# Performance work log

Hardware: AMD Instinct MI355X
Metric: run time of the kernel (lower is better)

The kernel has to match this reference:

```python
import jax, jax.numpy as jnp
import numpy as np

B, N, DIM, H, DH = 8, 1024, 512, 8, 64
INNER = H * DH
SCALE = DH ** -0.5


def setup_inputs() -> dict:
    key = jax.random.key(0)
    ks = jax.random.split(key, 9)
    s = 0.02
    return {
        "x": jax.random.normal(ks[0], (B, N, DIM), jnp.float32),
        "lidar": jax.random.normal(ks[1], (B, N, INNER), jnp.float32),
        "w_qkv": jax.random.normal(ks[2], (3 * INNER, DIM), jnp.float32) * s,
        "w_merge": jax.random.normal(ks[3], (DH, DH), jnp.float32) * s,
        "b_merge": jnp.zeros((DH,), jnp.float32),
        "w_out": jax.random.normal(ks[4], (DIM, INNER), jnp.float32) * s,
        "b_out": jnp.zeros((DIM,), jnp.float32),
        "conv_w": jax.random.normal(ks[5], (2,), jnp.float32) * 0.5,
        "conv_b": jnp.zeros((), jnp.float32),
    }


def _split_heads(t):  # [b, n, h*d] -> [b, h, n, d]
    b, n, _ = t.shape
    return t.reshape(b, n, H, DH).transpose(0, 2, 1, 3)


def reference(x, lidar, w_qkv, w_merge, b_merge, w_out, b_out, conv_w, conv_b):
    b, n, _ = x.shape
    qkv = x @ w_qkv.T  # [b, n, 3*inner]
    q, k, v = jnp.split(qkv, 3, axis=-1)
    q, k, v = _split_heads(q), _split_heads(k), _split_heads(v)
    lid = _split_heads(lidar)

    dots = jnp.einsum('bhid,bhjd->bhij', q, k) * SCALE
    lidar_sim = jnp.einsum('bhid,bhjd->bhij', lid, lid) * SCALE
    lidar_sim = jax.nn.softmax(lidar_sim, axis=-1)

    # 1x1 conv over 2 channels == learned linear blend of the two score maps
    mid = conv_w[0] * dots + conv_w[1] * lidar_sim + conv_b
    attn = jax.nn.softmax(mid, axis=-1)

    out = jnp.einsum('bhij,bhjd->bhid', attn, v)
    out = out @ w_merge.T + b_merge                  # per-head linear_merge
    out = out.transpose(0, 2, 1, 3).reshape(b, n, INNER)  # b h n d -> b n (h d)
    out = out @ w_out.T + b_out                      # to_out (dropout = identity)
    return (out, lidar)
```

## Files before the change

kernel.cpp:

```cpp
#include <hip/hip_runtime.h>
#include <hip/hip_bf16.h>

#define B_      8
#define N_      1024
#define DIM_    512
#define H_      8
#define DH_     64
#define INNER_  512
#define SCALE_  0.125f
#define LOG2E_  1.4426950408889634f

typedef __attribute__((ext_vector_type(8))) __bf16         bf16x8;
typedef __attribute__((ext_vector_type(8))) unsigned short ushort8;
typedef __attribute__((ext_vector_type(4))) float          f32x4;

union FragCast { ushort8 u; bf16x8 b; };
union FragU32  { unsigned int u[4]; bf16x8 b; };

__device__ inline bf16x8 ld_frag(const unsigned short* p) {
    FragCast f; f.u = *(const ushort8*)p; return f.b;
}

__device__ inline f32x4 mfma16(bf16x8 a, bf16x8 b, f32x4 c) {
    return __builtin_amdgcn_mfma_f32_16x16x32_bf16(a, b, c, 0, 0, 0);
}

__device__ inline float fexp2(float x) { return __builtin_amdgcn_exp2f(x); }

__device__ inline unsigned short f2bf(float x) {
    unsigned int u = __float_as_uint(x);
    unsigned int lsb = (u >> 16) & 1u;
    u += 0x7fffu + lsb;
    return (unsigned short)(u >> 16);
}

__device__ inline unsigned int pack_bf2(float hi, float lo) {
    return __builtin_amdgcn_perm(__float_as_uint(hi), __float_as_uint(lo), 0x07060302u);
}

__device__ inline void gl_lds(const unsigned short* g, unsigned short* l) {
    __builtin_amdgcn_global_load_lds(
        (const __attribute__((address_space(1))) unsigned int*)g,
        (__attribute__((address_space(3))) unsigned int*)l, 16, 0, 0);
}

#define BARF() do { asm volatile("" ::: "memory"); \
                    __builtin_amdgcn_s_barrier();  \
                    asm volatile("" ::: "memory"); } while (0)
#define WAITV(n) asm volatile("s_waitcnt vmcnt(" #n ")" ::: "memory")

#define KEEP8(x) do { FragU32 _k; _k.b = (x); \
    asm volatile("" :: "v"(_k.u[0]), "v"(_k.u[1]), "v"(_k.u[2]), "v"(_k.u[3])); } while (0)

__global__ __launch_bounds__(256) void k_convert(
    const float* __restrict__ x, const float* __restrict__ lidar,
    const float* __restrict__ wqkv, const float* __restrict__ wmerge,
    const float* __restrict__ wout,
    unsigned short* __restrict__ x_bf, unsigned short* __restrict__ lid_bf,
    float* __restrict__ out_lidar,
    unsigned short* __restrict__ wqkv_bf, unsigned short* __restrict__ wm_bf,
    unsigned short* __restrict__ wout_bf)
{
    const int bx = blockIdx.x, tid = threadIdx.x;
    const float* src; unsigned short* dst; bool isLid = false; long base;
    if (bx < 1024)      { src = x;      dst = x_bf;    base = (long)bx * 1024; }
    else if (bx < 2048) { src = lidar;  dst = lid_bf;  base = (long)(bx - 1024) * 1024; isLid = true; }
    else if (bx < 2240) { src = wqkv;   dst = wqkv_bf; base = (long)(bx - 2048) * 1024; }
    else if (bx < 2304) { src = wout;   dst = wout_bf; base = (long)(bx - 2240) * 1024; }
    else                { src = wmerge; dst = wm_bf;   base = 0; }
    for (int k = 0; k < 4; k++) {
        long j = base + k * 256 + tid;
        float4 v = ((const float4*)src)[j];
        ushort4 o;
        o.x = f2bf(v.x); o.y = f2bf(v.y); o.z = f2bf(v.z); o.w = f2bf(v.w);
        ((ushort4*)dst)[j] = o;
        if (isLid) ((float4*)out_lidar)[j] = v;
    }
}

__global__ __launch_bounds__(256) void k_gemm_qkv(
    const unsigned short* __restrict__ A, const unsigned short* __restrict__ Bm,
    unsigned short* __restrict__ C, unsigned short* __restrict__ vt,
    int M, int Nd, int K)
{
    __shared__ unsigned short sMem[128 * 136];
    unsigned short* sA = sMem;
    unsigned short* sB = sMem + 128 * 64;
    const int tid  = threadIdx.x;
    const int lane = tid & 63, wave = tid >> 6;
    const int q = lane >> 4, l15 = lane & 15, l7 = l15 & 7;
    const int xq0 = (q ^ l7) << 3, xq4 = ((q + 4) ^ l7) << 3;
    const int m0 = blockIdx.x * 128, n0 = blockIdx.y * 128;
    const int wm = (wave >> 1) * 64, wn = (wave & 1) * 64;
    f32x4 acc[4][4] = {};

    for (int k0 = 0; k0 < K; k0 += 64) {
        __syncthreads();
        for (int i = 0; i < 4; i++) {
            int c = i * 256 + tid;
            int row = c >> 3;
            int gcol = ((c & 7) ^ (row & 7)) << 3;
            gl_lds(&A[(long)(m0 + row) * K + k0 + gcol], &sA[c * 8]);
            gl_lds(&Bm[(long)(n0 + row) * K + k0 + gcol], &sB[c * 8]);
        }
        __syncthreads();
        for (int kk = 0; kk < 2; kk++) {
            const int xx = kk ? xq4 : xq0;
            bf16x8 af[4], bfr[4];
            for (int i = 0; i < 4; i++)
                af[i]  = ld_frag(&sA[(wm + i * 16 + l15) * 64 + xx]);
            for (int i = 0; i < 4; i++)
                bfr[i] = ld_frag(&sB[(wn + i * 16 + l15) * 64 + xx]);
            for (int mi = 0; mi < 4; mi++)
                for (int ni = 0; ni < 4; ni++)
                    acc[mi][ni] = mfma16(af[mi], bfr[ni], acc[mi][ni]);
        }
    }
    if (n0 < 1024) {
        for (int mi = 0; mi < 4; mi++)
            for (int ni = 0; ni < 4; ni++)
                for (int r = 0; r < 4; r++) {
                    int row = m0 + wm + mi * 16 + q * 4 + r;
                    int col = n0 + wn + ni * 16 + l15;
                    C[(long)row * Nd + col] = f2bf(acc[mi][ni][r]);
                }
    } else {
        __syncthreads();
        for (int mi = 0; mi < 4; mi++) {
            int t0 = wm + mi * 16 + q * 4;
            for (int ni = 0; ni < 4; ni++) {
                int f = wn + ni * 16 + l15;
                ushort4 o4;
                o4.x = f2bf(acc[mi][ni][0]); o4.y = f2bf(acc[mi][ni][1]);
                o4.z = f2bf(acc[mi][ni][2]); o4.w = f2bf(acc[mi][ni][3]);
                *(ushort4*)&sMem[f * 136 + t0] = o4;
            }
        }
        __syncthreads();
        const long fb = (long)(n0 - 1024) * (B_ * N_) + m0;
        for (int i = 0; i < 8; i++) {
            int g = i * 256 + tid;
            int f = g >> 4, grp = g & 15;
            int base = (grp >> 2) * 32 + (grp & 3) * 4;
            ushort4 a4 = *(const ushort4*)&sMem[f * 136 + base];
            ushort4 b4 = *(const ushort4*)&sMem[f * 136 + base + 16];
            ushort8 o8 = {a4.x, a4.y, a4.z, a4.w, b4.x, b4.y, b4.z, b4.w};
            *(ushort8*)&vt[fb + (long)f * (B_ * N_) + grp * 8] = o8;
        }
    }
}

__global__ __launch_bounds__(256) void k_gemm_out(
    const unsigned short* __restrict__ A, const unsigned short* __restrict__ Bm,
    const float* __restrict__ bias, float* __restrict__ C, int M, int Nd, int K)
{
    __shared__ unsigned short sA[128 * 64];
    __shared__ unsigned short sB[64 * 64];
    const int tid  = threadIdx.x;
    const int lane = tid & 63, wave = tid >> 6;
    const int q = lane >> 4, l15 = lane & 15, l7 = l15 & 7;
    const int xq0 = (q ^ l7) << 3, xq4 = ((q + 4) ^ l7) << 3;
    const int m0 = blockIdx.x * 128, n0 = blockIdx.y * 64;
    const int wm = (wave >> 1) * 64, wn = (wave & 1) * 32;
    f32x4 acc[4][2] = {};

    for (int k0 = 0; k0 < K; k0 += 64) {
        __syncthreads();
        for (int i = 0; i < 4; i++) {
            int c = i * 256 + tid;
            int row = c >> 3;
            int gcol = ((c & 7) ^ (row & 7)) << 3;
            gl_lds(&A[(long)(m0 + row) * K + k0 + gcol], &sA[c * 8]);
            if (i < 2)
                gl_lds(&Bm[(long)(n0 + row) * K + k0 + gcol], &sB[c * 8]);
        }
        __syncthreads();
        for (int kk = 0; kk < 2; kk++) {
            const int xx = kk ? xq4 : xq0;
            bf16x8 af[4], bfr[2];
            for (int i = 0; i < 4; i++)
                af[i]  = ld_frag(&sA[(wm + i * 16 + l15) * 64 + xx]);
            for (int i = 0; i < 2; i++)
                bfr[i] = ld_frag(&sB[(wn + i * 16 + l15) * 64 + xx]);
            for (int mi = 0; mi < 4; mi++)
                for (int ni = 0; ni < 2; ni++)
                    acc[mi][ni] = mfma16(af[mi], bfr[ni], acc[mi][ni]);
        }
    }
    for (int mi = 0; mi < 4; mi++)
        for (int ni = 0; ni < 2; ni++)
            for (int r = 0; r < 4; r++) {
                int row = m0 + wm + mi * 16 + q * 4 + r;
                int col = n0 + wn + ni * 16 + l15;
                C[(long)row * Nd + col] = acc[mi][ni][r] + bias[col];
            }
}


__device__ __forceinline__ void comp1(const unsigned short* smem, int SB,
                                      int a0, int a4,
                                      const bf16x8* lfq, float sc, float& rsl)
{
#pragma unroll
    for (int ns = 0; ns < 8; ns++) {
        f32x4 cv = {0.f, 0.f, 0.f, 0.f};
        cv = mfma16(ld_frag(&smem[SB + ns * 1024 + a0]), lfq[0], cv);
        cv = mfma16(ld_frag(&smem[SB + ns * 1024 + a4]), lfq[1], cv);
#pragma unroll
        for (int r = 0; r < 4; r++) rsl += fexp2(cv[r] * sc);
    }
}

__device__ __forceinline__ void comp2(const unsigned short* smem, int KB,
                                      int a0, int a4,
                                      const bf16x8* qf, const bf16x8* lfq,
                                      float k0c, float k2c, float k1, float sc,
                                      float& rs, f32x4* o)
{
#pragma unroll
    for (int ns2 = 0; ns2 < 2; ns2++) {
        FragU32 fa;
#pragma unroll
        for (int h2 = 0; h2 < 2; h2++) {
            const int ns = ns2 * 2 + h2;
            f32x4 a = {0.f, 0.f, 0.f, 0.f};
            a = mfma16(ld_frag(&smem[KB + ns * 1024 + a0]), qf[0], a);
            a = mfma16(ld_frag(&smem[KB + ns * 1024 + a4]), qf[1], a);
            f32x4 cv = {0.f, 0.f, 0.f, 0.f};
            cv = mfma16(ld_frag(&smem[KB + 4096 + ns * 1024 + a0]), lfq[0], cv);
            cv = mfma16(ld_frag(&smem[KB + 4096 + ns * 1024 + a4]), lfq[1], cv);
            float pv[4];
#pragma unroll
            for (int r = 0; r < 4; r++) {
                float els = fexp2(cv[r] * sc);
                float t = fmaf(k0c, a[r], k2c);
                t = fmaf(k1, els, t);
                pv[r] = fexp2(t);
                rs += pv[r];
            }
            fa.u[h2 * 2 + 0] = pack_bf2(pv[1], pv[0]);
            fa.u[h2 * 2 + 1] = pack_bf2(pv[3], pv[2]);
        }
        const int av = ns2 ? a4 : a0;
#pragma unroll
        for (int dt = 0; dt < 4; dt++)
            o[dt] = mfma16(fa.b, ld_frag(&smem[KB + 8192 + dt * 1024 + av]), o[dt]);
    }
}

__global__ __launch_bounds__(512) void k_flash(
    const unsigned short* __restrict__ qkv_bf, const unsigned short* __restrict__ lid_bf,
    const unsigned short* __restrict__ vt,
    const unsigned short* __restrict__ wm_bf, const float* __restrict__ b_merge,
    const float* __restrict__ conv_w, const float* __restrict__ conv_b,
    unsigned short* __restrict__ tmp_bf)
{
    __shared__ unsigned short smem[36864];
    __shared__ float sRS[8][16];

    const int tid = threadIdx.x, lane = tid & 63, wave = tid >> 6;
    const int q = lane >> 4, l15 = lane & 15, l7 = l15 & 7;
    const int xq0 = (q ^ l7) << 3, xq4 = ((q + 4) ^ l7) << 3;
    const int a0 = l15 * 64 + xq0, a4 = l15 * 64 + xq4;
    const int bh = blockIdx.x, ipair = blockIdx.y;
    const int b = bh >> 3, h = bh & 7;
    const int i0w = ipair * 128 + wave * 16;
    const long rowB = (long)b * N_;
    const int colh = h * DH_;
    const float k0c = conv_w[0] * SCALE_ * LOG2E_;
    const float k2c = conv_b[0] * LOG2E_;
    const float c1L = conv_w[1] * LOG2E_;
    const float sc = SCALE_ * LOG2E_;

    const int srow = tid >> 3;
    const int sgc  = ((tid & 7) ^ (srow & 7)) << 3;
    unsigned short* sd = &smem[tid * 8];
    const unsigned short* gK = &qkv_bf[(rowB + srow) * 1536 + 512 + colh + sgc];
    const unsigned short* gL = &lid_bf[(rowB + srow) * INNER_ + colh + sgc];
    const unsigned short* gV = &vt[(long)(colh + srow) * (B_ * N_) + rowB + sgc];
    const unsigned short* gL1a = &lid_bf[(rowB + srow) * INNER_ + colh + sgc];
    const unsigned short* gL1b = &lid_bf[(rowB + 64 + srow) * INNER_ + colh + sgc];

    bf16x8 qf[2], lfq[2];
#pragma unroll
    for (int ks = 0; ks < 2; ks++) {
        qf[ks]  = ld_frag(&qkv_bf[(rowB + i0w + l15) * 1536 + colh + ks * 32 + q * 8]);
        lfq[ks] = ld_frag(&lid_bf[(rowB + i0w + l15) * INNER_ + colh + ks * 32 + q * 8]);
    }
    KEEP8(qf[0]); KEEP8(qf[1]); KEEP8(lfq[0]); KEEP8(lfq[1]);
    WAITV(0);

#define ISS1(off) do { gl_lds(gL1a, sd + (off)); gl_lds(gL1b, sd + (off) + 4096); \
                       gL1a += 128 * INNER_; gL1b += 128 * INNER_; } while (0)
#define ISS2(off) do { gl_lds(gK, sd + (off)); gl_lds(gL, sd + (off) + 4096); \
                       gl_lds(gV, sd + (off) + 8192); \
                       gK += 64 * 1536; gL += 64 * INNER_; gV += 64; } while (0)

    float rsl = 0.f;
    ISS1(0); ISS1(8192);
    int cb = 0;
    for (int s = 0; s < 6; s++) {
        int dst = cb + 16384; if (dst >= 24576) dst -= 24576;
        ISS1(dst);
        WAITV(4); BARF();
        __builtin_amdgcn_s_setprio(1);
        comp1(smem, cb, a0, a4, lfq, sc, rsl);
        __builtin_amdgcn_s_setprio(0);
        BARF();
        cb += 8192; if (cb >= 24576) cb = 0;
    }
    WAITV(2); BARF();
    __builtin_amdgcn_s_setprio(1);
    comp1(smem, cb, a0, a4, lfq, sc, rsl);
    __builtin_amdgcn_s_setprio(0);
    BARF();
    cb += 8192; if (cb >= 24576) cb = 0;
    WAITV(0); BARF();
    __builtin_amdgcn_s_setprio(1);
    comp1(smem, cb, a0, a4, lfq, sc, rsl);
    __builtin_amdgcn_s_setprio(0);
    BARF();

    ISS2(0); ISS2(12288);
    rsl += __shfl_xor(rsl, 16);
    rsl += __shfl_xor(rsl, 32);
    const float k1 = c1L / rsl;
    float rs = 0.f;
    f32x4 o[4] = {};

    cb = 0;
    for (int s = 0; s < 14; s++) {
        int dst = cb + 24576; if (dst >= 36864) dst -= 36864;
        ISS2(dst);
        WAITV(6); BARF();
        __builtin_amdgcn_s_setprio(1);
        comp2(smem, cb, a0, a4, qf, lfq, k0c, k2c, k1, sc, rs, o);
        __builtin_amdgcn_s_setprio(0);
        BARF();
        cb += 12288; if (cb >= 36864) cb = 0;
    }
    WAITV(3); BARF();
    __builtin_amdgcn_s_setprio(1);
    comp2(smem, cb, a0, a4, qf, lfq, k0c, k2c, k1, sc, rs, o);
    __builtin_amdgcn_s_setprio(0);
    BARF();
    cb += 12288; if (cb >= 36864) cb = 0;
    WAITV(0); BARF();
    __builtin_amdgcn_s_setprio(1);
    comp2(smem, cb, a0, a4, qf, lfq, k0c, k2c, k1, sc, rs, o);
    __builtin_amdgcn_s_setprio(0);
    BARF();
#undef ISS1
#undef ISS2

    rs += __shfl_xor(rs, 16);
    rs += __shfl_xor(rs, 32);
    if (q == 0) sRS[wave][l15] = rs;
    float invr[4];
    for (int r = 0; r < 4; r++) invr[r] = 1.f / sRS[wave][q * 4 + r];

    unsigned short* pO = &smem[wave * 16 * 72];
#pragma unroll
    for (int dt = 0; dt < 4; dt++)
        for (int r = 0; r < 4; r++)
            pO[(q * 4 + r) * 72 + dt * 16 + l15] = f2bf(o[dt][r] * invr[r]);

    f32x4 mo[4] = {};
#pragma unroll
    for (int ks = 0; ks < 2; ks++) {
        bf16x8 af = ld_frag(&pO[l15 * 72 + ks * 32 + q * 8]);
#pragma unroll
        for (int ns = 0; ns < 4; ns++) {
            bf16x8 wf = ld_frag(&wm_bf[(ns * 16 + l15) * 64 + ks * 32 + q * 8]);
            mo[ns] = mfma16(af, wf, mo[ns]);
        }
    }
#pragma unroll
    for (int ns = 0; ns < 4; ns++) {
        float bm = b_merge[ns * 16 + l15];
        for (int r = 0; r < 4; r++) {
            long row = rowB + i0w + q * 4 + r;
            tmp_bf[row * INNER_ + colh + ns * 16 + l15] = f2bf(mo[ns][r] + bm);
        }
    }
}

extern "C" void kernel_launch(void* const* d_in, const int* in_sizes, int n_in,
                              void* d_out, int out_size, void* d_ws, size_t ws_size,
                              hipStream_t stream) {
    const float* x       = (const float*)d_in[0];
    const float* lidar   = (const float*)d_in[1];
    const float* w_qkv   = (const float*)d_in[2];
    const float* w_merge = (const float*)d_in[3];
    const float* b_merge = (const float*)d_in[4];
    const float* w_out   = (const float*)d_in[5];
    const float* b_out   = (const float*)d_in[6];
    const float* conv_w  = (const float*)d_in[7];
    const float* conv_b  = (const float*)d_in[8];

    float* out0      = (float*)d_out;
    float* out_lidar = out0 + (long)B_ * N_ * INNER_;

    size_t off = 0;
    auto carve = [&](size_t bytes) {
        void* p = (char*)d_ws + off;
        off += (bytes + 255) & ~(size_t)255;
        return p;
    };
    unsigned short* qkv_bf  = (unsigned short*)carve((size_t)B_ * N_ * 3 * INNER_ * 2);
    unsigned short* lid_bf  = (unsigned short*)carve((size_t)B_ * N_ * INNER_ * 2);
    unsigned short* x_bf    = (unsigned short*)carve((size_t)B_ * N_ * DIM_ * 2);
    unsigned short* wqkv_bf = (unsigned short*)carve((size_t)3 * INNER_ * DIM_ * 2);
    unsigned short* wout_bf = (unsigned short*)carve((size_t)DIM_ * INNER_ * 2);
    unsigned short* wm_bf   = (unsigned short*)carve((size_t)DH_ * DH_ * 2);
    unsigned short* tmp_bf  = (unsigned short*)carve((size_t)B_ * N_ * INNER_ * 2);
    unsigned short* vt_bf   = (unsigned short*)carve((size_t)INNER_ * B_ * N_ * 2);

    k_convert<<<2305, 256, 0, stream>>>(x, lidar, w_qkv, w_merge, w_out,
                                        x_bf, lid_bf, out_lidar,
                                        wqkv_bf, wm_bf, wout_bf);

    k_gemm_qkv<<<dim3(64, 12), 256, 0, stream>>>(
        x_bf, wqkv_bf, qkv_bf, vt_bf, B_ * N_, 3 * INNER_, DIM_);

    k_flash<<<dim3(64, 8), 512, 0, stream>>>(
        qkv_bf, lid_bf, vt_bf, wm_bf, b_merge, conv_w, conv_b, tmp_bf);

    k_gemm_out<<<dim3(64, 8), 256, 0, stream>>>(
        tmp_bf, wout_bf, b_out, out0, B_ * N_, DIM_, INNER_);
}
```

Measured before the change: 180.9 us.

## Unroll triple-buffered attention loops, drop trailing barrier, use constant LDS offsets

Both pipelined passes (lidar row-sum pass and main attention pass) are fully unrolled. The buffer offsets become template constants, so LDS addresses fold at compile time. Each step now waits, synchronises once, computes, and only then issues the async load two stages ahead into the buffer freed in the previous step. This removes one workgroup barrier per step and the runtime ring-index arithmetic. The trade-off is larger code, and loads now issue after compute rather than before, which shortens the effective prefetch lead.

```diff
diff --git a/kernel.cpp b/kernel.cpp
--- a/kernel.cpp
+++ b/kernel.cpp
@@ -197,8 +197,8 @@
 }
 
 
-__device__ __forceinline__ void comp1(const unsigned short* smem, int SB,
-                                      int a0, int a4,
+template <int SB>
+__device__ __forceinline__ void comp1(const unsigned short* smem, int a0, int a4,
                                       const bf16x8* lfq, float sc, float& rsl)
 {
 #pragma unroll
@@ -211,8 +211,8 @@
     }
 }
 
-__device__ __forceinline__ void comp2(const unsigned short* smem, int KB,
-                                      int a0, int a4,
+template <int KB>
+__device__ __forceinline__ void comp2(const unsigned short* smem, int a0, int a4,
                                       const bf16x8* qf, const bf16x8* lfq,
                                       float k0c, float k2c, float k1, float sc,
                                       float& rs, f32x4* o)
@@ -298,29 +298,23 @@
 
     float rsl = 0.f;
     ISS1(0); ISS1(8192);
-    int cb = 0;
-    for (int s = 0; s < 6; s++) {
-        int dst = cb + 16384; if (dst >= 24576) dst -= 24576;
-        ISS1(dst);
-        WAITV(4); BARF();
+#pragma unroll
+    for (int t = 0; t < 8; t++) {
+        if (t < 7) { WAITV(2); } else { WAITV(0); }
+        BARF();
         __builtin_amdgcn_s_setprio(1);
-        comp1(smem, cb, a0, a4, lfq, sc, rsl);
+        if      (t % 3 == 0) comp1<0>    (smem, a0, a4, lfq, sc, rsl);
+        else if (t % 3 == 1) comp1<8192> (smem, a0, a4, lfq, sc, rsl);
+        else                 comp1<16384>(smem, a0, a4, lfq, sc, rsl);
         __builtin_amdgcn_s_setprio(0);
-        BARF();
-        cb += 8192; if (cb >= 24576) cb = 0;
-    }
-    WAITV(2); BARF();
-    __builtin_amdgcn_s_setprio(1);
-    comp1(smem, cb, a0, a4, lfq, sc, rsl);
-    __builtin_amdgcn_s_setprio(0);
+        if (t + 2 < 8) {
+            if      ((t + 2) % 3 == 0) ISS1(0);
+            else if ((t + 2) % 3 == 1) ISS1(8192);
+            else                       ISS1(16384);
+        }
+    }
+
     BARF();
-    cb += 8192; if (cb >= 24576) cb = 0;
-    WAITV(0); BARF();
-    __builtin_amdgcn_s_setprio(1);
-    comp1(smem, cb, a0, a4, lfq, sc, rsl);
-    __builtin_amdgcn_s_setprio(0);
-    BARF();
-
     ISS2(0); ISS2(12288);
     rsl += __shfl_xor(rsl, 16);
     rsl += __shfl_xor(rsl, 32);
@@ -328,30 +322,24 @@
     float rs = 0.f;
     f32x4 o[4] = {};
 
-    cb = 0;
-    for (int s = 0; s < 14; s++) {
-        int dst = cb + 24576; if (dst >= 36864) dst -= 36864;
-        ISS2(dst);
-        WAITV(6); BARF();
+#pragma unroll
+    for (int t = 0; t < 16; t++) {
+        if (t < 15) { WAITV(3); } else { WAITV(0); }
+        BARF();
         __builtin_amdgcn_s_setprio(1);
-        comp2(smem, cb, a0, a4, qf, lfq, k0c, k2c, k1, sc, rs, o);
+        if      (t % 3 == 0) comp2<0>    (smem, a0, a4, qf, lfq, k0c, k2c, k1, sc, rs, o);
+        else if (t % 3 == 1) comp2<12288>(smem, a0, a4, qf, lfq, k0c, k2c, k1, sc, rs, o);
+        else                 comp2<24576>(smem, a0, a4, qf, lfq, k0c, k2c, k1, sc, rs, o);
         __builtin_amdgcn_s_setprio(0);
-        BARF();
-        cb += 12288; if (cb >= 36864) cb = 0;
-    }
-    WAITV(3); BARF();
-    __builtin_amdgcn_s_setprio(1);
-    comp2(smem, cb, a0, a4, qf, lfq, k0c, k2c, k1, sc, rs, o);
-    __builtin_amdgcn_s_setprio(0);
-    BARF();
-    cb += 12288; if (cb >= 36864) cb = 0;
-    WAITV(0); BARF();
-    __builtin_amdgcn_s_setprio(1);
-    comp2(smem, cb, a0, a4, qf, lfq, k0c, k2c, k1, sc, rs, o);
-    __builtin_amdgcn_s_setprio(0);
-    BARF();
+        if (t + 2 < 16) {
+            if      ((t + 2) % 3 == 0) ISS2(0);
+            else if ((t + 2) % 3 == 1) ISS2(12288);
+            else                       ISS2(24576);
+        }
+    }
 #undef ISS1
 #undef ISS2
+    BARF();
 
     rs += __shfl_xor(rs, 16);
     rs += __shfl_xor(rs, 32);
```

New measurement: 179.1 us. No clear change (-1.0%).
